# Performance work log

Measured on AMD Instinct MI355X. Metric: run time of the kernel, lower is better.

Reference implementation:

```python
import jax, jax.numpy as jnp
import numpy as np

N_MB = 4  # number of micro-behavior buckets; C = N_MB**2 + 1

def setup_inputs() -> dict:
    key = jax.random.key(0)
    k_q, k_k, k_b, k_w, k_a = jax.random.split(key, 5)
    b, h, S, d = 8, 8, 512, 64
    C = N_MB * N_MB + 1
    return {
        "query": jax.random.normal(k_q, (b, h, S, d), dtype=jnp.float32),
        "key": jax.random.normal(k_k, (b, h, S, d), dtype=jnp.float32),
        "b_seq": jax.random.randint(k_b, (b, S), 0, N_MB + 1, dtype=jnp.int32),
        "W1": jax.random.normal(k_w, (N_MB, h, d, d), dtype=jnp.float32) * 0.02,
        "alpha1": jax.random.normal(k_a, (C, N_MB, h), dtype=jnp.float32) * 0.02,
    }

def reference(query, key, b_seq, W1, alpha1):
    # bucket-pair index per (i, j) token pair; 0 if either token is padding
    bi = b_seq[:, :, None]  # [b, S, 1]
    bj = b_seq[:, None, :]  # [b, 1, S]
    b_mat = ((bi - 1) * N_MB + bj) * (bi * bj != 0).astype(jnp.int32)  # [b, S, S]
    # mix the n_mb base bilinear weights into C per-bucket-pair matrices
    W1_ = jnp.einsum('Bhmn,CBh->Chmn', W1, jax.nn.softmax(alpha1, axis=1))
    # full bilinear score for every bucket-pair class C (the wasteful part)
    att_all = jnp.einsum('bhim,Chmn,bhjn->bhijC', query, W1_, key)  # [b,h,S,S,C]
    # select the score matching each pair's bucket index
    idx = b_mat[:, None, :, :, None].astype(jnp.int32)  # [b,1,S,S,1] -> broadcast over h
    idx = jnp.broadcast_to(idx, att_all.shape[:4] + (1,))
    scores = jnp.take_along_axis(att_all, idx, axis=4)[..., 0]  # [b,h,S,S]
    return scores
```

## Files before the change

kernel.cpp:

```cpp
#include <hip/hip_runtime.h>
#include <stdint.h>

#define NB 4
#define NC 17
#define HH 8
#define SS 512
#define DD 64
#define CT 32

typedef __attribute__((ext_vector_type(8))) short bf16x8;
typedef __attribute__((ext_vector_type(4))) float f32x4;

#define WS_W1   0
#define WS_RIDX 1114112
#define WS_GST  (WS_RIDX + 16384)

__device__ __forceinline__ unsigned short f2bf(float f) {
  unsigned int x; __builtin_memcpy(&x, &f, 4);
  return (unsigned short)((x + 0x7fff + ((x >> 16) & 1)) >> 16);
}
__device__ __forceinline__ bf16x8 cvt8(const float* p) {
  float4 a = *(const float4*)p;
  float4 b = *(const float4*)(p + 4);
  union { bf16x8 v; unsigned short u[8]; } t;
  t.u[0] = f2bf(a.x); t.u[1] = f2bf(a.y); t.u[2] = f2bf(a.z); t.u[3] = f2bf(a.w);
  t.u[4] = f2bf(b.x); t.u[5] = f2bf(b.y); t.u[6] = f2bf(b.z); t.u[7] = f2bf(b.w);
  return t.v;
}

__global__ __launch_bounds__(256) void k_prep(const int* __restrict__ bseq,
                                              const float* __restrict__ W1,
                                              const float* __restrict__ alpha,
                                              int* __restrict__ ridx,
                                              int* __restrict__ gst,
                                              unsigned short* __restrict__ W1mbf) {
  int tid = threadIdx.x;
  if (blockIdx.x < 8) {
    int b = blockIdx.x;
    __shared__ int cnt[5], base[6], cur[5];
    if (tid < 5) cnt[tid] = 0;
    __syncthreads();
    for (int j = tid; j < SS; j += blockDim.x) atomicAdd(&cnt[bseq[b * SS + j]], 1);
    __syncthreads();
    if (tid == 0) {
      base[0] = 0;
      for (int k = 0; k < 5; k++) base[k + 1] = base[k] + cnt[k];
      for (int k = 0; k < 6; k++) gst[b * 6 + k] = base[k];
    }
    __syncthreads();
    if (tid < 5) cur[tid] = base[tid];
    __syncthreads();
    for (int j = tid; j < SS; j += blockDim.x) {
      int p = atomicAdd(&cur[bseq[b * SS + j]], 1);
      ridx[b * SS + p] = j;
    }
  } else {
    int cb = blockIdx.x - 8;
    int c = cb >> 3, hh = cb & 7;
    __shared__ float sm[NB];
    if (tid == 0) {
      float a[NB], mx = -1e30f;
      for (int B = 0; B < NB; B++) { a[B] = alpha[(c * NB + B) * HH + hh]; mx = fmaxf(mx, a[B]); }
      float s = 0.f;
      for (int B = 0; B < NB; B++) { a[B] = __expf(a[B] - mx); s += a[B]; }
      for (int B = 0; B < NB; B++) sm[B] = a[B] / s;
    }
    __syncthreads();
    float s0 = sm[0], s1 = sm[1], s2 = sm[2], s3 = sm[3];
    for (int idx = tid; idx < DD * DD; idx += blockDim.x) {
      float v = W1[((0 * HH + hh) * DD * DD) + idx] * s0 +
                W1[((1 * HH + hh) * DD * DD) + idx] * s1 +
                W1[((2 * HH + hh) * DD * DD) + idx] * s2 +
                W1[((3 * HH + hh) * DD * DD) + idx] * s3;
      W1mbf[((size_t)(c * HH + hh)) * DD * DD + idx] = f2bf(v);
    }
  }
}

__global__ __launch_bounds__(256) void k_fused(const float* __restrict__ query,
                                               const float* __restrict__ key,
                                               const int* __restrict__ bseq,
                                               const unsigned short* __restrict__ W1mbf,
                                               const int* __restrict__ ridx,
                                               const int* __restrict__ gst,
                                               float* __restrict__ out) {
  int bx = blockIdx.x;
  int bh = bx & 63, jt = bx >> 6;
  int b = bh >> 3, h = bh & 7;
  int j0 = jt * CT;
  int tid = threadIdx.x, wave = tid >> 6, lane = tid & 63;
  int quad = lane >> 4, l16 = lane & 15;

  __shared__ __align__(16) unsigned short Tl[5][CT][72];
  __shared__ int ord[CT], lgs[6], cnt[5], cur[5];
  __shared__ int p1list[40], p2list[40];
  __shared__ int n1s[5], n2s[5], n1b[5], n2b[5];
  __shared__ int n1tot, n2tot;

  if (tid < 5) cnt[tid] = 0;
  __syncthreads();
  int mybj = 0;
  if (tid < CT) { mybj = bseq[b * SS + j0 + tid]; atomicAdd(&cnt[mybj], 1); }
  __syncthreads();
  if (tid == 0) {
    lgs[0] = 0;
    for (int a = 0; a < 5; a++) lgs[a + 1] = lgs[a] + cnt[a];
  }
  __syncthreads();
  if (tid < 5) cur[tid] = lgs[tid];
  __syncthreads();
  if (tid < CT) ord[atomicAdd(&cur[mybj], 1)] = tid;
  if (tid < 5) {
    int a = tid;
    int tiles = (lgs[a + 1] - lgs[a] + 15) >> 4;
    n1s[a] = tiles * ((a == 0) ? 1 : 5);
    int gs = gst[b * 6 + a], ge = gst[b * 6 + a + 1];
    n2s[a] = (ge - gs + 15) >> 4;
  }
  __syncthreads();
  if (tid == 0) {
    int a0 = 0, a1 = 0;
    for (int a = 0; a < 5; a++) {
      n1b[a] = a0; a0 += n1s[a];
      n2b[a] = a1; a1 += n2s[a];
    }
    n1tot = a0; n2tot = a1;
  }
  __syncthreads();
  if (tid < 5) {
    int a = tid;
    int ls = lgs[a], le = lgs[a + 1];
    int w = n1b[a];
    for (int t0 = ls; t0 < le; t0 += 16) {
      if (a == 0) {
        p1list[w++] = t0 | (le << 5) | (1 << 19);
      } else {
        for (int B = 0; B < 5; B++) {
          int c = (B == 0) ? 0 : (B - 1) * NB + a;
          p1list[w++] = t0 | (le << 5) | (c << 11) | (B << 16);
        }
      }
    }
    int gs = gst[b * 6 + a], ge = gst[b * 6 + a + 1];
    w = n2b[a];
    for (int p0 = gs; p0 < ge; p0 += 16)
      p2list[w++] = p0 | (ge << 10) | (a << 20);
  }
  __syncthreads();

  for (int idx = wave; idx < n1tot; idx += 4) {
    int e = p1list[idx];
    int t0 = e & 31, le = (e >> 5) & 63, c = (e >> 11) & 31, B = (e >> 16) & 7;
    int bc = (e >> 19) & 1;
    const unsigned short* Wc = W1mbf + ((size_t)(c * HH + h) << 12);
    int p = t0 + l16; if (p > le - 1) p = le - 1;
    int cl = ord[p];
    const float* kp = &key[((size_t)(bh * SS + j0 + cl)) * DD + quad * 8];
    bf16x8 af0 = cvt8(kp);
    bf16x8 af1 = cvt8(kp + 32);
    int cr[4];
#pragma unroll
    for (int reg = 0; reg < 4; reg++) {
      int pr = t0 + quad * 4 + reg;
      cr[reg] = (pr < le) ? ord[pr] : -1;
    }
#pragma unroll
    for (int nt = 0; nt < 4; nt++) {
      const unsigned short* wp = &Wc[(nt * 16 + l16) * DD + quad * 8];
      bf16x8 b0 = *(const bf16x8*)wp;
      bf16x8 b1 = *(const bf16x8*)(wp + 32);
      f32x4 acc = {0.f, 0.f, 0.f, 0.f};
      acc = __builtin_amdgcn_mfma_f32_16x16x32_bf16(af0, b0, acc, 0, 0, 0);
      acc = __builtin_amdgcn_mfma_f32_16x16x32_bf16(af1, b1, acc, 0, 0, 0);
#pragma unroll
      for (int reg = 0; reg < 4; reg++) {
        if (cr[reg] >= 0) {
          unsigned short v = f2bf(acc[reg]);
          if (bc) {
#pragma unroll
            for (int Bw = 0; Bw < 5; Bw++) Tl[Bw][cr[reg]][nt * 16 + l16] = v;
          } else {
            Tl[B][cr[reg]][nt * 16 + l16] = v;
          }
        }
      }
    }
  }
  __syncthreads();

  for (int idx = wave; idx < n2tot; idx += 4) {
    int e = p2list[idx];
    int p0 = e & 1023, ge = (e >> 10) & 1023, B = e >> 20;
    int p = p0 + l16; if (p > ge - 1) p = ge - 1;
    int r = ridx[b * SS + p];
    const float* qp = &query[((size_t)(bh * SS + r)) * DD + quad * 8];
    bf16x8 af0 = cvt8(qp);
    bf16x8 af1 = cvt8(qp + 32);
    int rr[4];
#pragma unroll
    for (int reg = 0; reg < 4; reg++) {
      int pr = p0 + quad * 4 + reg;
      rr[reg] = (pr < ge) ? ridx[b * SS + pr] : -1;
    }
#pragma unroll
    for (int ct = 0; ct < 2; ct++) {
      const unsigned short* tp = &Tl[B][ct * 16 + l16][quad * 8];
      bf16x8 b0 = *(const bf16x8*)tp;
      bf16x8 b1 = *(const bf16x8*)(tp + 32);
      f32x4 acc = {0.f, 0.f, 0.f, 0.f};
      acc = __builtin_amdgcn_mfma_f32_16x16x32_bf16(af0, b0, acc, 0, 0, 0);
      acc = __builtin_amdgcn_mfma_f32_16x16x32_bf16(af1, b1, acc, 0, 0, 0);
#pragma unroll
      for (int reg = 0; reg < 4; reg++)
        if (rr[reg] >= 0)
          out[((size_t)(bh * SS + rr[reg])) * SS + j0 + ct * 16 + l16] = acc[reg];
    }
  }
}

extern "C" void kernel_launch(void* const* d_in, const int* in_sizes, int n_in,
                              void* d_out, int out_size, void* d_ws, size_t ws_size,
                              hipStream_t stream) {
  const float* q = (const float*)d_in[0];
  const float* k = (const float*)d_in[1];
  const int* bseq = (const int*)d_in[2];
  const float* W1 = (const float*)d_in[3];
  const float* alpha = (const float*)d_in[4];
  float* out = (float*)d_out;
  char* ws = (char*)d_ws;
  unsigned short* W1mbf = (unsigned short*)(ws + WS_W1);
  int* ridx = (int*)(ws + WS_RIDX);
  int* gst = (int*)(ws + WS_GST);

  hipLaunchKernelGGL(k_prep, dim3(8 + NC * HH), dim3(256), 0, stream,
                     bseq, W1, alpha, ridx, gst, W1mbf);
  hipLaunchKernelGGL(k_fused, dim3(64 * (SS / CT)), dim3(256), 0, stream,
                     q, k, bseq, W1mbf, ridx, gst, out);
}
```

Before: 138.7 us.

## Widen column tile to 64, use 512-thread blocks, process two query tiles per wave

```diff
diff --git a/kernel.cpp b/kernel.cpp
--- a/kernel.cpp
+++ b/kernel.cpp
@@ -6,7 +6,7 @@
 #define HH 8
 #define SS 512
 #define DD 64
-#define CT 32
+#define CT 64
 
 typedef __attribute__((ext_vector_type(8))) short bf16x8;
 typedef __attribute__((ext_vector_type(4))) float f32x4;
@@ -19,9 +19,7 @@
   unsigned int x; __builtin_memcpy(&x, &f, 4);
   return (unsigned short)((x + 0x7fff + ((x >> 16) & 1)) >> 16);
 }
-__device__ __forceinline__ bf16x8 cvt8(const float* p) {
-  float4 a = *(const float4*)p;
-  float4 b = *(const float4*)(p + 4);
+__device__ __forceinline__ bf16x8 cvt8(float4 a, float4 b) {
   union { bf16x8 v; unsigned short u[8]; } t;
   t.u[0] = f2bf(a.x); t.u[1] = f2bf(a.y); t.u[2] = f2bf(a.z); t.u[3] = f2bf(a.w);
   t.u[4] = f2bf(b.x); t.u[5] = f2bf(b.y); t.u[6] = f2bf(b.z); t.u[7] = f2bf(b.w);
@@ -77,13 +75,13 @@
   }
 }
 
-__global__ __launch_bounds__(256) void k_fused(const float* __restrict__ query,
-                                               const float* __restrict__ key,
-                                               const int* __restrict__ bseq,
-                                               const unsigned short* __restrict__ W1mbf,
-                                               const int* __restrict__ ridx,
-                                               const int* __restrict__ gst,
-                                               float* __restrict__ out) {
+__global__ __launch_bounds__(512, 4) void k_fused(const float* __restrict__ query,
+                                                  const float* __restrict__ key,
+                                                  const int* __restrict__ bseq,
+                                                  const unsigned short* __restrict__ W1mbf,
+                                                  const int* __restrict__ ridx,
+                                                  const int* __restrict__ gst,
+                                                  float* __restrict__ out) {
   int bx = blockIdx.x;
   int bh = bx & 63, jt = bx >> 6;
   int b = bh >> 3, h = bh & 7;
@@ -94,8 +92,7 @@
   __shared__ __align__(16) unsigned short Tl[5][CT][72];
   __shared__ int ord[CT], lgs[6], cnt[5], cur[5];
   __shared__ int p1list[40], p2list[40];
-  __shared__ int n1s[5], n2s[5], n1b[5], n2b[5];
-  __shared__ int n1tot, n2tot;
+  __shared__ int n1s[5], n1b[5], n1tot, n2tot;
 
   if (tid < 5) cnt[tid] = 0;
   __syncthreads();
@@ -110,21 +107,15 @@
   if (tid < 5) cur[tid] = lgs[tid];
   __syncthreads();
   if (tid < CT) ord[atomicAdd(&cur[mybj], 1)] = tid;
-  if (tid < 5) {
-    int a = tid;
-    int tiles = (lgs[a + 1] - lgs[a] + 15) >> 4;
-    n1s[a] = tiles * ((a == 0) ? 1 : 5);
-    int gs = gst[b * 6 + a], ge = gst[b * 6 + a + 1];
-    n2s[a] = (ge - gs + 15) >> 4;
-  }
+  if (tid < 5) n1s[tid] = ((lgs[tid + 1] - lgs[tid] + 15) >> 4) * ((tid == 0) ? 1 : 5);
   __syncthreads();
   if (tid == 0) {
-    int a0 = 0, a1 = 0;
-    for (int a = 0; a < 5; a++) {
-      n1b[a] = a0; a0 += n1s[a];
-      n2b[a] = a1; a1 += n2s[a];
-    }
-    n1tot = a0; n2tot = a1;
+    int a0 = 0;
+    for (int a = 0; a < 5; a++) { n1b[a] = a0; a0 += n1s[a]; }
+    n1tot = a0;
+    int a1 = 0;
+    for (int a = 0; a < 5; a++) a1 += (gst[b * 6 + a + 1] - gst[b * 6 + a] + 15) >> 4;
+    n2tot = a1;
   }
   __syncthreads();
   if (tid < 5) {
@@ -133,31 +124,34 @@
     int w = n1b[a];
     for (int t0 = ls; t0 < le; t0 += 16) {
       if (a == 0) {
-        p1list[w++] = t0 | (le << 5) | (1 << 19);
+        p1list[w++] = t0 | (le << 6) | (1 << 21);
       } else {
         for (int B = 0; B < 5; B++) {
           int c = (B == 0) ? 0 : (B - 1) * NB + a;
-          p1list[w++] = t0 | (le << 5) | (c << 11) | (B << 16);
+          p1list[w++] = t0 | (le << 6) | (c << 13) | (B << 18);
         }
       }
     }
+    int w2 = 0;
+    for (int aa = 0; aa < a; aa++) w2 += (gst[b * 6 + aa + 1] - gst[b * 6 + aa] + 15) >> 4;
     int gs = gst[b * 6 + a], ge = gst[b * 6 + a + 1];
-    w = n2b[a];
     for (int p0 = gs; p0 < ge; p0 += 16)
-      p2list[w++] = p0 | (ge << 10) | (a << 20);
-  }
-  __syncthreads();
-
-  for (int idx = wave; idx < n1tot; idx += 4) {
+      p2list[w2++] = p0 | (ge << 10) | (a << 20);
+  }
+  __syncthreads();
+
+  for (int idx = wave; idx < n1tot; idx += 8) {
     int e = p1list[idx];
-    int t0 = e & 31, le = (e >> 5) & 63, c = (e >> 11) & 31, B = (e >> 16) & 7;
-    int bc = (e >> 19) & 1;
+    int t0 = e & 63, le = (e >> 6) & 127, c = (e >> 13) & 31, B = (e >> 18) & 7;
+    int bc = (e >> 21) & 1;
     const unsigned short* Wc = W1mbf + ((size_t)(c * HH + h) << 12);
     int p = t0 + l16; if (p > le - 1) p = le - 1;
     int cl = ord[p];
     const float* kp = &key[((size_t)(bh * SS + j0 + cl)) * DD + quad * 8];
-    bf16x8 af0 = cvt8(kp);
-    bf16x8 af1 = cvt8(kp + 32);
+    float4 ka = *(const float4*)kp, kb = *(const float4*)(kp + 4);
+    float4 kc = *(const float4*)(kp + 32), kd = *(const float4*)(kp + 36);
+    bf16x8 af0 = cvt8(ka, kb);
+    bf16x8 af1 = cvt8(kc, kd);
     int cr[4];
 #pragma unroll
     for (int reg = 0; reg < 4; reg++) {
@@ -188,32 +182,55 @@
   }
   __syncthreads();
 
-  for (int idx = wave; idx < n2tot; idx += 4) {
-    int e = p2list[idx];
-    int p0 = e & 1023, ge = (e >> 10) & 1023, B = e >> 20;
-    int p = p0 + l16; if (p > ge - 1) p = ge - 1;
-    int r = ridx[b * SS + p];
-    const float* qp = &query[((size_t)(bh * SS + r)) * DD + quad * 8];
-    bf16x8 af0 = cvt8(qp);
-    bf16x8 af1 = cvt8(qp + 32);
-    int rr[4];
+  for (int i0 = wave * 2; i0 < n2tot; i0 += 16) {
+    int e0 = p2list[i0];
+    bool has1 = (i0 + 1) < n2tot;
+    int e1 = has1 ? p2list[i0 + 1] : e0;
+
+    int p0a = e0 & 1023, gea = (e0 >> 10) & 1023, Ba = e0 >> 20;
+    int p0b = e1 & 1023, geb = (e1 >> 10) & 1023, Bb = e1 >> 20;
+
+    int pa = p0a + l16; if (pa > gea - 1) pa = gea - 1;
+    int pb = p0b + l16; if (pb > geb - 1) pb = geb - 1;
+    int ra = ridx[b * SS + pa];
+    int rb = ridx[b * SS + pb];
+    const float* qa = &query[((size_t)(bh * SS + ra)) * DD + quad * 8];
+    const float* qb = &query[((size_t)(bh * SS + rb)) * DD + quad * 8];
+    float4 a0 = *(const float4*)qa, a1 = *(const float4*)(qa + 4);
+    float4 a2 = *(const float4*)(qa + 32), a3 = *(const float4*)(qa + 36);
+    float4 b0_ = *(const float4*)qb, b1_ = *(const float4*)(qb + 4);
+    float4 b2_ = *(const float4*)(qb + 32), b3_ = *(const float4*)(qb + 36);
+    bf16x8 afa0 = cvt8(a0, a1), afa1 = cvt8(a2, a3);
+    bf16x8 afb0 = cvt8(b0_, b1_), afb1 = cvt8(b2_, b3_);
+
+    int rra[4], rrb[4];
 #pragma unroll
     for (int reg = 0; reg < 4; reg++) {
-      int pr = p0 + quad * 4 + reg;
-      rr[reg] = (pr < ge) ? ridx[b * SS + pr] : -1;
-    }
-#pragma unroll
-    for (int ct = 0; ct < 2; ct++) {
-      const unsigned short* tp = &Tl[B][ct * 16 + l16][quad * 8];
-      bf16x8 b0 = *(const bf16x8*)tp;
-      bf16x8 b1 = *(const bf16x8*)(tp + 32);
-      f32x4 acc = {0.f, 0.f, 0.f, 0.f};
-      acc = __builtin_amdgcn_mfma_f32_16x16x32_bf16(af0, b0, acc, 0, 0, 0);
-      acc = __builtin_amdgcn_mfma_f32_16x16x32_bf16(af1, b1, acc, 0, 0, 0);
-#pragma unroll
-      for (int reg = 0; reg < 4; reg++)
-        if (rr[reg] >= 0)
-          out[((size_t)(bh * SS + rr[reg])) * SS + j0 + ct * 16 + l16] = acc[reg];
+      int pra = p0a + quad * 4 + reg;
+      rra[reg] = (pra < gea) ? ridx[b * SS + pra] : -1;
+      int prb = p0b + quad * 4 + reg;
+      rrb[reg] = (has1 && prb < geb) ? ridx[b * SS + prb] : -1;
+    }
+#pragma unroll
+    for (int ct = 0; ct < CT / 16; ct++) {
+      const unsigned short* tpa = &Tl[Ba][ct * 16 + l16][quad * 8];
+      const unsigned short* tpb = &Tl[Bb][ct * 16 + l16][quad * 8];
+      bf16x8 ba0 = *(const bf16x8*)tpa;
+      bf16x8 ba1 = *(const bf16x8*)(tpa + 32);
+      bf16x8 bb0 = *(const bf16x8*)tpb;
+      bf16x8 bb1 = *(const bf16x8*)(tpb + 32);
+      f32x4 acca = {0.f, 0.f, 0.f, 0.f}, accb = {0.f, 0.f, 0.f, 0.f};
+      acca = __builtin_amdgcn_mfma_f32_16x16x32_bf16(afa0, ba0, acca, 0, 0, 0);
+      accb = __builtin_amdgcn_mfma_f32_16x16x32_bf16(afb0, bb0, accb, 0, 0, 0);
+      acca = __builtin_amdgcn_mfma_f32_16x16x32_bf16(afa1, ba1, acca, 0, 0, 0);
+      accb = __builtin_amdgcn_mfma_f32_16x16x32_bf16(afb1, bb1, accb, 0, 0, 0);
+#pragma unroll
+      for (int reg = 0; reg < 4; reg++) {
+        if (rra[reg] >= 0)
+          out[((size_t)(bh * SS + rra[reg])) * SS + j0 + ct * 16 + l16] = acca[reg];
+        if (rrb[reg] >= 0)
+          out[((size_t)(bh * SS + rrb[reg])) * SS + j0 + ct * 16 + l16] = accb[reg];
+      }
     }
   }
 }
@@ -234,6 +251,6 @@
 
   hipLaunchKernelGGL(k_prep, dim3(8 + NC * HH), dim3(256), 0, stream,
                      bseq, W1, alpha, ridx, gst, W1mbf);
-  hipLaunchKernelGGL(k_fused, dim3(64 * (SS / CT)), dim3(256), 0, stream,
+  hipLaunchKernelGGL(k_fused, dim3(64 * (SS / CT)), dim3(512), 0, stream,
                      q, k, bseq, W1mbf, ridx, gst, out);
 }
```

New measurement: 119.8 us. 13.6% less time.
